# Performance work log

Measured on AMD Instinct MI355X. Metric: run time of the kernel, lower is better.

Reference implementation:

```python
import jax, jax.numpy as jnp
import numpy as np

B, R, D, P = 32, 512, 256, 5532  # images, rois/image, feat dim, num_pids
NEG_INF = -1e30

def setup_inputs() -> dict:
    key = jax.random.key(0)
    k1, k2, k3 = jax.random.split(key, 3)
    inputs = jax.random.normal(k1, (B * R, D), dtype=jnp.float32)
    cls_scores = jax.random.uniform(k2, (B * R, 1), dtype=jnp.float32)
    roi_label = jax.random.randint(k3, (B, R), 0, P + 1)  # 0 = background -> label -1
    return {"inputs": inputs, "cls_scores": cls_scores, "roi_label": roi_label}

def reference(inputs, cls_scores, roi_label):
    x = (inputs * cls_scores).reshape(B, R, D)          # scale features by cls score
    label = roi_label - 1                               # [B,R], -1 = background
    valid = label >= 0                                  # keep labeled ROIs only
    lbl = jnp.where(valid, label, 0)

    # per-image per-pid mean prototypes via one segmented reduction
    seg = (jnp.arange(B)[:, None] * P + lbl).reshape(-1)             # [B*R]
    w = valid.reshape(-1).astype(x.dtype)
    sums = jax.ops.segment_sum(x.reshape(-1, D) * w[:, None], seg, num_segments=B * P)
    counts = jax.ops.segment_sum(w, seg, num_segments=B * P)          # [B*P]
    proto = sums / jnp.maximum(counts, 1.0)[:, None]
    proto = proto / jnp.maximum(jnp.linalg.norm(proto, axis=-1, keepdims=True), 1e-12)
    proto = jax.lax.stop_gradient(proto).reshape(B, P, D)            # .detach() in torch
    present = (counts > 0).reshape(B, P)                              # unique labels per image

    # project each ROI feature onto its image's prototypes
    logits = jnp.einsum('brd,bpd->brp', x, proto)                     # [B,R,P]
    logits = jnp.where(present[:, None, :], logits, NEG_INF)          # softmax over unique labels only
    logp = jax.nn.log_softmax(logits, axis=-1)
    nll = -jnp.take_along_axis(logp, lbl[..., None], axis=-1)[..., 0] # [B,R]
    nll = jnp.where(valid, nll, 0.0)
    n_valid = jnp.maximum(jnp.sum(valid).astype(x.dtype), 1.0)
    return jnp.sum(nll) / n_valid
```

## Files before the change

kernel.cpp:

```cpp
#include <hip/hip_runtime.h>
#include <math.h>

#define Bn 32
#define Rn 512
#define Dn 256
#define Pn 5532
#define MAXU 512
#define NEGBIG -3.0e38f

typedef short short8 __attribute__((ext_vector_type(8)));
typedef short short4v __attribute__((ext_vector_type(4)));
typedef float floatx4 __attribute__((ext_vector_type(4)));

#define COUNTS_OFF   0
#define NLL_OFF      (Bn*Pn)
#define TICKET_OFF   (NLL_OFF + 1)
#define ZERO_WORDS   (TICKET_OFF + 3)
#define XBF_OFF      ZERO_WORDS
#define XBF_WORDS    (Bn*Rn*Dn/2)
#define PBF_OFF      (XBF_OFF + XBF_WORDS)
#define PBF_WORDS    (Bn*MAXU*Dn/2)
#define CMAP_OFF     (PBF_OFF + PBF_WORDS)
#define CCNT_OFF     (CMAP_OFF + Bn*Pn)
#define CURS_OFF     (CCNT_OFF + Bn*MAXU)
#define RLIST_OFF    (CURS_OFF + Bn*MAXU)
#define NUNIQ_OFF    (RLIST_OFF + Bn*Rn)
#define NVALID_OFF   (NUNIQ_OFF + 32)
#define MPART_OFF    (NVALID_OFF + 32)
#define SPART_OFF    (MPART_OFF + Bn*Rn*4)
#define DLBL_OFF     (SPART_OFF + Bn*Rn*4)

__device__ __forceinline__ unsigned short bf16r(float f) {
    union { float f; unsigned int u; } c; c.f = f;
    return (unsigned short)((c.u + 0x7FFFu + ((c.u >> 16) & 1u)) >> 16);
}

__device__ __forceinline__ void async16(void* lds, const void* g) {
    auto* l3 = reinterpret_cast<__attribute__((address_space(3))) unsigned int*>(
                   reinterpret_cast<size_t>(lds));
    auto* g1 = reinterpret_cast<const __attribute__((address_space(1))) unsigned int*>(
                   reinterpret_cast<size_t>(g));
    __builtin_amdgcn_global_load_lds(g1, l3, 16, 0, 0);
}

__global__ __launch_bounds__(256) void k_prep(const float* __restrict__ inputs,
                                              const float* __restrict__ cls,
                                              const int* __restrict__ roi_label,
                                              unsigned short* __restrict__ xbf,
                                              int* __restrict__ counts) {
    int i8 = blockIdx.x * 256 + threadIdx.x;
    if (i8 < Bn * Rn) {
        int b = i8 >> 9;
        int lbl = roi_label[i8] - 1;
        if (lbl >= 0) atomicAdd(&counts[b * Pn + lbl], 1);
    }
    int e = i8 * 8;
    int row = e >> 8;
    float cw = cls[row];
    float4 v0 = *(const float4*)&inputs[e];
    float4 v1 = *(const float4*)&inputs[e + 4];
    short8 o;
    o[0] = (short)bf16r(v0.x * cw); o[1] = (short)bf16r(v0.y * cw);
    o[2] = (short)bf16r(v0.z * cw); o[3] = (short)bf16r(v0.w * cw);
    o[4] = (short)bf16r(v1.x * cw); o[5] = (short)bf16r(v1.y * cw);
    o[6] = (short)bf16r(v1.z * cw); o[7] = (short)bf16r(v1.w * cw);
    *(short8*)&xbf[e] = o;
}

__global__ __launch_bounds__(1024) void k_compact(
    const int* __restrict__ roi_label, const int* __restrict__ counts,
    int* __restrict__ nuniq, int* __restrict__ cmap, int* __restrict__ ccnt,
    int* __restrict__ cursor, int* __restrict__ rlist, int* __restrict__ nvalid_arr) {
    const int b = blockIdx.x;
    const int t = threadIdx.x;
    const int lane = t & 63, wid = t >> 6;
    __shared__ int wpres[16], wcnt[16];
    __shared__ int cmap_lds[Pn];
    __shared__ int curs_lds[MAXU];
    int basePres = 0, baseCnt = 0;
    for (int i0 = 0; i0 < Pn; i0 += 1024) {
        int i = i0 + t;
        int cnt = (i < Pn) ? counts[b * Pn + i] : 0;
        bool pres = cnt > 0;
        unsigned long long mask = __ballot(pres);
        int pfx_pres = __popcll(mask & ((1ULL << lane) - 1ULL));
        int v = cnt;
        #pragma unroll
        for (int off = 1; off < 64; off <<= 1) {
            int u = __shfl_up(v, off);
            if (lane >= off) v += u;
        }
        int pfx_cnt = v - cnt;
        if (lane == 63) { wpres[wid] = __popcll(mask); wcnt[wid] = v; }
        __syncthreads();
        int woffP = 0, totP = 0, woffC = 0, totC = 0;
        #pragma unroll
        for (int w = 0; w < 16; ++w) {
            int p = wpres[w], c = wcnt[w];
            if (w < wid) { woffP += p; woffC += c; }
            totP += p; totC += c;
        }
        if (pres) {
            int c = basePres + woffP + pfx_pres;
            cmap_lds[i] = c;
            cmap[b * Pn + i] = c;
            ccnt[b * MAXU + c] = cnt;
            curs_lds[c] = baseCnt + woffC + pfx_cnt;
        }
        basePres += totP; baseCnt += totC;
        __syncthreads();
    }
    if (t < Rn) {
        int lbl = roi_label[b * Rn + t] - 1;
        if (lbl >= 0) {
            int c = cmap_lds[lbl];
            int pos = atomicAdd(&curs_lds[c], 1);
            rlist[b * Rn + pos] = t;
        }
    }
    __syncthreads();
    if (t < MAXU && t < basePres)
        cursor[b * MAXU + t] = curs_lds[t];
    if (t == 0) { nuniq[b] = basePres; nvalid_arr[b] = baseCnt; }
}

__global__ __launch_bounds__(64) void k_proto(
    const float* __restrict__ inputs, const float* __restrict__ cls,
    const int* __restrict__ nuniq, const int* __restrict__ ccnt,
    const int* __restrict__ cursor, const int* __restrict__ rlist,
    unsigned short* __restrict__ pbf) {
    int slot = blockIdx.x;
    int b = slot >> 9;
    int c = slot & (MAXU - 1);
    if (c >= nuniq[b]) return;
    int cnt = ccnt[slot];
    int start = cursor[slot] - cnt;
    int t = threadIdx.x;
    float4 acc = make_float4(0.f, 0.f, 0.f, 0.f);
    for (int k = 0; k < cnt; ++k) {
        int r = rlist[b * Rn + start + k];
        float cw = cls[b * Rn + r];
        float4 v = *(const float4*)&inputs[(size_t)(b * Rn + r) * Dn + t * 4];
        acc.x += v.x * cw; acc.y += v.y * cw; acc.z += v.z * cw; acc.w += v.w * cw;
    }
    float inv = 1.0f / (float)cnt;
    acc.x *= inv; acc.y *= inv; acc.z *= inv; acc.w *= inv;
    float ss = acc.x*acc.x + acc.y*acc.y + acc.z*acc.z + acc.w*acc.w;
    #pragma unroll
    for (int off = 32; off > 0; off >>= 1) ss += __shfl_xor(ss, off);
    float scale = 1.0f / fmaxf(sqrtf(ss), 1e-12f);
    short4v o;
    o[0] = (short)bf16r(acc.x * scale); o[1] = (short)bf16r(acc.y * scale);
    o[2] = (short)bf16r(acc.z * scale); o[3] = (short)bf16r(acc.w * scale);
    *(short4v*)&pbf[(size_t)slot * Dn + t * 4] = o;
}

#define TRr 128
#define TCc 128
#define KCk 32

__global__ __launch_bounds__(256, 3) void k_loss(
    const unsigned short* __restrict__ xbf, const unsigned short* __restrict__ pbf,
    const int* __restrict__ roi_label, const int* __restrict__ cmap,
    const int* __restrict__ nuniq,
    float* __restrict__ mpart, float* __restrict__ spart,
    float* __restrict__ dlbl_arr)
{
    __shared__ __align__(16) unsigned short xs[2][TRr * KCk];
    __shared__ __align__(16) unsigned short ps[2][TCc * KCk];
    __shared__ int lblc[TRr];
    __shared__ float mw[4][TRr], sw[4][TRr];

    const int t = threadIdx.x;
    const int lane = t & 63, w = t >> 6;
    const int q = lane >> 4, r15 = lane & 15;
    const int b = blockIdx.z;
    const int pc = blockIdx.y;
    const int roiBase = blockIdx.x * TRr;
    const int U = nuniq[b];
    if (pc * TCc >= U) return;

    if (t < TRr) {
        int lbl = roi_label[b * Rn + roiBase + t] - 1;
        lblc[t] = (lbl >= 0) ? cmap[b * Pn + lbl] : -1;
    }

    int xrow[2], xg[2], prow[2], pg[2];
    #pragma unroll
    for (int cc = 0; cc < 2; ++cc) {
        int s = (w + cc * 4) * 64 + lane;
        xrow[cc] = s >> 2; xg[cc] = (s & 3) ^ ((xrow[cc] >> 1) & 3);
        prow[cc] = s >> 2; pg[cc] = xg[cc];
    }

    #define ISSUE(kc, buf)                                                         \
        do {                                                                       \
            async16(&xs[buf][w * 512],                                             \
                    xbf + (size_t)(b * Rn + roiBase + xrow[0]) * Dn                \
                        + (kc) * KCk + xg[0] * 8);                                 \
            async16(&xs[buf][(w + 4) * 512],                                       \
                    xbf + (size_t)(b * Rn + roiBase + xrow[1]) * Dn                \
                        + (kc) * KCk + xg[1] * 8);                                 \
            async16(&ps[buf][w * 512],                                             \
                    pbf + (size_t)(b * MAXU + pc * TCc + prow[0]) * Dn             \
                        + (kc) * KCk + pg[0] * 8);                                 \
            async16(&ps[buf][(w + 4) * 512],                                       \
                    pbf + (size_t)(b * MAXU + pc * TCc + prow[1]) * Dn             \
                        + (kc) * KCk + pg[1] * 8);                                 \
        } while (0)

    ISSUE(0, 0);

    floatx4 acc[8][2];
    #pragma unroll
    for (int mt = 0; mt < 8; ++mt)
        #pragma unroll
        for (int nt = 0; nt < 2; ++nt) acc[mt][nt] = (floatx4)0.f;

    for (int kc = 0; kc < Dn / KCk; ++kc) {
        const int cur = kc & 1;
        __syncthreads();
        if (kc < Dn / KCk - 1) ISSUE(kc + 1, cur ^ 1);

        short8 bb[2];
        #pragma unroll
        for (int nt = 0; nt < 2; ++nt) {
            int row = w * 32 + nt * 16 + r15;
            int off = row * KCk + ((q ^ ((row >> 1) & 3)) * 8);
            bb[nt] = *(const short8*)&ps[cur][off];
        }
        #pragma unroll
        for (int mt = 0; mt < 8; ++mt) {
            int row = mt * 16 + r15;
            int off = row * KCk + ((q ^ ((row >> 1) & 3)) * 8);
            short8 a = *(const short8*)&xs[cur][off];
            acc[mt][0] = __builtin_amdgcn_mfma_f32_16x16x32_bf16(a, bb[0], acc[mt][0], 0, 0, 0);
            acc[mt][1] = __builtin_amdgcn_mfma_f32_16x16x32_bf16(a, bb[1], acc[mt][1], 0, 0, 0);
        }
    }

    const int c0 = pc * TCc + w * 32 + r15;
    const int c1 = c0 + 16;
    const bool v0 = c0 < U, v1 = c1 < U;
    #pragma unroll
    for (int mt = 0; mt < 8; ++mt)
        #pragma unroll
        for (int reg = 0; reg < 4; ++reg) {
            int mloc = mt * 16 + q * 4 + reg;
            float d0 = acc[mt][0][reg], d1 = acc[mt][1][reg];
            int lc = lblc[mloc];
            if (v0 && c0 == lc) dlbl_arr[b * Rn + roiBase + mloc] = d0;
            if (v1 && c1 == lc) dlbl_arr[b * Rn + roiBase + mloc] = d1;
            float M = fmaxf(v0 ? d0 : NEGBIG, v1 ? d1 : NEGBIG);
            #pragma unroll
            for (int off = 1; off < 16; off <<= 1) M = fmaxf(M, __shfl_xor(M, off));
            float s = (v0 ? __expf(d0 - M) : 0.f) + (v1 ? __expf(d1 - M) : 0.f);
            #pragma unroll
            for (int off = 1; off < 16; off <<= 1) s += __shfl_xor(s, off);
            if (r15 == 0) { mw[w][mloc] = M; sw[w][mloc] = s; }
        }
    __syncthreads();

    if (t < TRr) {
        float M = fmaxf(fmaxf(mw[0][t], mw[1][t]), fmaxf(mw[2][t], mw[3][t]));
        float s = 0.f;
        #pragma unroll
        for (int wv = 0; wv < 4; ++wv) s += sw[wv][t] * __expf(mw[wv][t] - M);
        int roi = b * Rn + roiBase + t;
        mpart[roi * 4 + pc] = M;
        spart[roi * 4 + pc] = s;
    }
    #undef ISSUE
}

__global__ __launch_bounds__(256) void k_merge(
    const int* __restrict__ roi_label, const int* __restrict__ nuniq,
    const float* __restrict__ mpart, const float* __restrict__ spart,
    const float* __restrict__ dlbl_arr, float* __restrict__ nll_sum,
    int* __restrict__ ticket, const int* __restrict__ nvalid_arr,
    float* __restrict__ out)
{
    __shared__ float wsum[4];
    int roi = blockIdx.x * 256 + threadIdx.x;
    int b = roi >> 9;
    int lbl = roi_label[roi] - 1;
    float v = 0.f;
    if (lbl >= 0) {
        int U = nuniq[b];
        int nch = (U + TCc - 1) / TCc;
        float m = NEGBIG, s = 0.f;
        for (int pc = 0; pc < nch; ++pc) {
            float om = mpart[roi * 4 + pc], os = spart[roi * 4 + pc];
            float M = fmaxf(m, om);
            s = s * __expf(m - M) + os * __expf(om - M);
            m = M;
        }
        v = m + __logf(s) - dlbl_arr[roi];
    }
    #pragma unroll
    for (int off = 1; off < 64; off <<= 1) v += __shfl_xor(v, off);
    int lane = threadIdx.x & 63, wid = threadIdx.x >> 6;
    if (lane == 0) wsum[wid] = v;
    __syncthreads();
    if (threadIdx.x == 0) {
        atomicAdd(nll_sum, wsum[0] + wsum[1] + wsum[2] + wsum[3]);
        __threadfence();
        int tk = atomicAdd(ticket, 1);
        if (tk == gridDim.x - 1) {
            __threadfence();
            int s = 0;
            #pragma unroll
            for (int bb = 0; bb < Bn; ++bb) s += nvalid_arr[bb];
            out[0] = nll_sum[0] / fmaxf((float)s, 1.0f);
        }
    }
}

extern "C" void kernel_launch(void* const* d_in, const int* in_sizes, int n_in,
                              void* d_out, int out_size, void* d_ws, size_t ws_size,
                              hipStream_t stream) {
    const float* inputs = (const float*)d_in[0];
    const float* cls    = (const float*)d_in[1];
    const int*   roi    = (const int*)d_in[2];
    float* out = (float*)d_out;

    float* wsf = (float*)d_ws;
    int*   wsi = (int*)d_ws;
    int*   counts = wsi + COUNTS_OFF;
    float* nll    = wsf + NLL_OFF;
    int*   ticket = wsi + TICKET_OFF;
    unsigned short* xbf = (unsigned short*)(wsi + XBF_OFF);
    unsigned short* pbf = (unsigned short*)(wsi + PBF_OFF);
    int*   cmap   = wsi + CMAP_OFF;
    int*   ccnt   = wsi + CCNT_OFF;
    int*   cursor = wsi + CURS_OFF;
    int*   rlist  = wsi + RLIST_OFF;
    int*   nuniq  = wsi + NUNIQ_OFF;
    int*   nvalid = wsi + NVALID_OFF;
    float* mpart  = wsf + MPART_OFF;
    float* spart  = wsf + SPART_OFF;
    float* dlbl   = wsf + DLBL_OFF;

    hipMemsetAsync(d_ws, 0, (size_t)ZERO_WORDS * 4, stream);
    k_prep   <<<(Bn*Rn*Dn)/(256*8), 256, 0, stream>>>(inputs, cls, roi, xbf, counts);
    k_compact<<<Bn, 1024, 0, stream>>>(roi, counts, nuniq, cmap, ccnt, cursor, rlist, nvalid);
    k_proto  <<<Bn*MAXU, 64, 0, stream>>>(inputs, cls, nuniq, ccnt, cursor, rlist, pbf);
    dim3 g(Rn / TRr, 4, Bn);
    k_loss   <<<g, 256, 0, stream>>>(xbf, pbf, roi, cmap, nuniq, mpart, spart, dlbl);
    k_merge  <<<(Bn*Rn)/256, 256, 0, stream>>>(roi, nuniq, mpart, spart, dlbl, nll,
                                               ticket, nvalid, out);
}
```

Measured before the change: 115.6 us.

## Fuse prep and compaction, drop memset and atomics, single-block final merge

Merges the bf16 conversion and label compaction into one launch. Compaction blocks now count labels in LDS instead of through global atomics, so the hipMemset of the counts array goes away. The proto kernel processes 8 slots per block to cut block count. The merge becomes a single 1024-thread block that reduces without atomics or a ticket. Removing two launches and the memset should shrink fixed overhead, but the single-block merge serializes 16K ROIs onto one CU and the fused kernel uses large LDS for its conversion blocks.

```diff
diff --git a/kernel.cpp b/kernel.cpp
--- a/kernel.cpp
+++ b/kernel.cpp
@@ -12,23 +12,19 @@
 typedef short short4v __attribute__((ext_vector_type(4)));
 typedef float floatx4 __attribute__((ext_vector_type(4)));
 
-#define COUNTS_OFF   0
-#define NLL_OFF      (Bn*Pn)
-#define TICKET_OFF   (NLL_OFF + 1)
-#define ZERO_WORDS   (TICKET_OFF + 3)
-#define XBF_OFF      ZERO_WORDS
-#define XBF_WORDS    (Bn*Rn*Dn/2)
-#define PBF_OFF      (XBF_OFF + XBF_WORDS)
-#define PBF_WORDS    (Bn*MAXU*Dn/2)
-#define CMAP_OFF     (PBF_OFF + PBF_WORDS)
-#define CCNT_OFF     (CMAP_OFF + Bn*Pn)
-#define CURS_OFF     (CCNT_OFF + Bn*MAXU)
-#define RLIST_OFF    (CURS_OFF + Bn*MAXU)
-#define NUNIQ_OFF    (RLIST_OFF + Bn*Rn)
-#define NVALID_OFF   (NUNIQ_OFF + 32)
-#define MPART_OFF    (NVALID_OFF + 32)
-#define SPART_OFF    (MPART_OFF + Bn*Rn*4)
-#define DLBL_OFF     (SPART_OFF + Bn*Rn*4)
+#define XBF_OFF    0
+#define XBF_WORDS  (Bn*Rn*Dn/2)
+#define PBF_OFF    (XBF_OFF + XBF_WORDS)
+#define PBF_WORDS  (Bn*MAXU*Dn/2)
+#define CMAP_OFF   (PBF_OFF + PBF_WORDS)
+#define CCNT_OFF   (CMAP_OFF + Bn*Pn)
+#define CURS_OFF   (CCNT_OFF + Bn*MAXU)
+#define RLIST_OFF  (CURS_OFF + Bn*MAXU)
+#define NUNIQ_OFF  (RLIST_OFF + Bn*Rn)
+#define NVALID_OFF (NUNIQ_OFF + 32)
+#define MPART_OFF  (NVALID_OFF + 32)
+#define SPART_OFF  (MPART_OFF + Bn*Rn*4)
+#define DLBL_OFF   (SPART_OFF + Bn*Rn*4)
 
 __device__ __forceinline__ unsigned short bf16r(float f) {
     union { float f; unsigned int u; } c; c.f = f;
@@ -43,44 +39,51 @@
     __builtin_amdgcn_global_load_lds(g1, l3, 16, 0, 0);
 }
 
-__global__ __launch_bounds__(256) void k_prep(const float* __restrict__ inputs,
-                                              const float* __restrict__ cls,
-                                              const int* __restrict__ roi_label,
-                                              unsigned short* __restrict__ xbf,
-                                              int* __restrict__ counts) {
-    int i8 = blockIdx.x * 256 + threadIdx.x;
-    if (i8 < Bn * Rn) {
-        int b = i8 >> 9;
-        int lbl = roi_label[i8] - 1;
-        if (lbl >= 0) atomicAdd(&counts[b * Pn + lbl], 1);
-    }
-    int e = i8 * 8;
-    int row = e >> 8;
-    float cw = cls[row];
-    float4 v0 = *(const float4*)&inputs[e];
-    float4 v1 = *(const float4*)&inputs[e + 4];
-    short8 o;
-    o[0] = (short)bf16r(v0.x * cw); o[1] = (short)bf16r(v0.y * cw);
-    o[2] = (short)bf16r(v0.z * cw); o[3] = (short)bf16r(v0.w * cw);
-    o[4] = (short)bf16r(v1.x * cw); o[5] = (short)bf16r(v1.y * cw);
-    o[6] = (short)bf16r(v1.z * cw); o[7] = (short)bf16r(v1.w * cw);
-    *(short8*)&xbf[e] = o;
-}
-
-__global__ __launch_bounds__(1024) void k_compact(
-    const int* __restrict__ roi_label, const int* __restrict__ counts,
-    int* __restrict__ nuniq, int* __restrict__ cmap, int* __restrict__ ccnt,
-    int* __restrict__ cursor, int* __restrict__ rlist, int* __restrict__ nvalid_arr) {
-    const int b = blockIdx.x;
+__global__ __launch_bounds__(1024) void k1_prep_compact(
+    const float* __restrict__ inputs, const float* __restrict__ cls,
+    const int* __restrict__ roi_label,
+    unsigned short* __restrict__ xbf,
+    int* __restrict__ cmap, int* __restrict__ ccnt, int* __restrict__ cursor,
+    int* __restrict__ rlist, int* __restrict__ nuniq, int* __restrict__ nvalid_arr)
+{
+    const int flat = blockIdx.x;
     const int t = threadIdx.x;
-    const int lane = t & 63, wid = t >> 6;
-    __shared__ int wpres[16], wcnt[16];
+
+    __shared__ int cnt_lds[Pn];
     __shared__ int cmap_lds[Pn];
     __shared__ int curs_lds[MAXU];
+    __shared__ int wpres[16], wcnt[16];
+
+    if (flat >= 32) {
+        int g = (flat - 32) * 1024 + t;
+        int e = g * 8;
+        int row = e >> 8;
+        float cw = cls[row];
+        float4 v0 = *(const float4*)&inputs[e];
+        float4 v1 = *(const float4*)&inputs[e + 4];
+        short8 o;
+        o[0] = (short)bf16r(v0.x * cw); o[1] = (short)bf16r(v0.y * cw);
+        o[2] = (short)bf16r(v0.z * cw); o[3] = (short)bf16r(v0.w * cw);
+        o[4] = (short)bf16r(v1.x * cw); o[5] = (short)bf16r(v1.y * cw);
+        o[6] = (short)bf16r(v1.z * cw); o[7] = (short)bf16r(v1.w * cw);
+        *(short8*)&xbf[e] = o;
+        return;
+    }
+
+    const int b = flat;
+    const int lane = t & 63, wid = t >> 6;
+    for (int i = t; i < Pn; i += 1024) cnt_lds[i] = 0;
+    __syncthreads();
+    if (t < Rn) {
+        int lbl = roi_label[b * Rn + t] - 1;
+        if (lbl >= 0) atomicAdd(&cnt_lds[lbl], 1);
+    }
+    __syncthreads();
+
     int basePres = 0, baseCnt = 0;
     for (int i0 = 0; i0 < Pn; i0 += 1024) {
         int i = i0 + t;
-        int cnt = (i < Pn) ? counts[b * Pn + i] : 0;
+        int cnt = (i < Pn) ? cnt_lds[i] : 0;
         bool pres = cnt > 0;
         unsigned long long mask = __ballot(pres);
         int pfx_pres = __popcll(mask & ((1ULL << lane) - 1ULL));
@@ -124,42 +127,45 @@
     if (t == 0) { nuniq[b] = basePres; nvalid_arr[b] = baseCnt; }
 }
 
-__global__ __launch_bounds__(64) void k_proto(
+__global__ __launch_bounds__(64) void k2_proto(
     const float* __restrict__ inputs, const float* __restrict__ cls,
     const int* __restrict__ nuniq, const int* __restrict__ ccnt,
     const int* __restrict__ cursor, const int* __restrict__ rlist,
-    unsigned short* __restrict__ pbf) {
-    int slot = blockIdx.x;
-    int b = slot >> 9;
-    int c = slot & (MAXU - 1);
-    if (c >= nuniq[b]) return;
-    int cnt = ccnt[slot];
-    int start = cursor[slot] - cnt;
+    unsigned short* __restrict__ pbf)
+{
     int t = threadIdx.x;
-    float4 acc = make_float4(0.f, 0.f, 0.f, 0.f);
-    for (int k = 0; k < cnt; ++k) {
-        int r = rlist[b * Rn + start + k];
-        float cw = cls[b * Rn + r];
-        float4 v = *(const float4*)&inputs[(size_t)(b * Rn + r) * Dn + t * 4];
-        acc.x += v.x * cw; acc.y += v.y * cw; acc.z += v.z * cw; acc.w += v.w * cw;
-    }
-    float inv = 1.0f / (float)cnt;
-    acc.x *= inv; acc.y *= inv; acc.z *= inv; acc.w *= inv;
-    float ss = acc.x*acc.x + acc.y*acc.y + acc.z*acc.z + acc.w*acc.w;
-    #pragma unroll
-    for (int off = 32; off > 0; off >>= 1) ss += __shfl_xor(ss, off);
-    float scale = 1.0f / fmaxf(sqrtf(ss), 1e-12f);
-    short4v o;
-    o[0] = (short)bf16r(acc.x * scale); o[1] = (short)bf16r(acc.y * scale);
-    o[2] = (short)bf16r(acc.z * scale); o[3] = (short)bf16r(acc.w * scale);
-    *(short4v*)&pbf[(size_t)slot * Dn + t * 4] = o;
+    int s0 = blockIdx.x * 8;
+    for (int s = s0; s < s0 + 8; ++s) {
+        int b = s >> 9;
+        int c = s & (MAXU - 1);
+        if (c >= nuniq[b]) continue;
+        int cnt = ccnt[s];
+        int start = cursor[s] - cnt;
+        float4 acc = make_float4(0.f, 0.f, 0.f, 0.f);
+        for (int k = 0; k < cnt; ++k) {
+            int r = rlist[b * Rn + start + k];
+            float cw = cls[b * Rn + r];
+            float4 v = *(const float4*)&inputs[(size_t)(b * Rn + r) * Dn + t * 4];
+            acc.x += v.x * cw; acc.y += v.y * cw; acc.z += v.z * cw; acc.w += v.w * cw;
+        }
+        float inv = 1.0f / (float)cnt;
+        acc.x *= inv; acc.y *= inv; acc.z *= inv; acc.w *= inv;
+        float ss = acc.x*acc.x + acc.y*acc.y + acc.z*acc.z + acc.w*acc.w;
+        #pragma unroll
+        for (int off = 32; off > 0; off >>= 1) ss += __shfl_xor(ss, off);
+        float scale = 1.0f / fmaxf(sqrtf(ss), 1e-12f);
+        short4v o;
+        o[0] = (short)bf16r(acc.x * scale); o[1] = (short)bf16r(acc.y * scale);
+        o[2] = (short)bf16r(acc.z * scale); o[3] = (short)bf16r(acc.w * scale);
+        *(short4v*)&pbf[(size_t)s * Dn + t * 4] = o;
+    }
 }
 
 #define TRr 128
 #define TCc 128
 #define KCk 32
 
-__global__ __launch_bounds__(256, 3) void k_loss(
+__global__ __launch_bounds__(256, 3) void k3_loss(
     const unsigned short* __restrict__ xbf, const unsigned short* __restrict__ pbf,
     const int* __restrict__ roi_label, const int* __restrict__ cmap,
     const int* __restrict__ nuniq,
@@ -185,12 +191,11 @@
         lblc[t] = (lbl >= 0) ? cmap[b * Pn + lbl] : -1;
     }
 
-    int xrow[2], xg[2], prow[2], pg[2];
+    int xrow[2], xg[2];
     #pragma unroll
     for (int cc = 0; cc < 2; ++cc) {
         int s = (w + cc * 4) * 64 + lane;
         xrow[cc] = s >> 2; xg[cc] = (s & 3) ^ ((xrow[cc] >> 1) & 3);
-        prow[cc] = s >> 2; pg[cc] = xg[cc];
     }
 
     #define ISSUE(kc, buf)                                                         \
@@ -202,11 +207,11 @@
                     xbf + (size_t)(b * Rn + roiBase + xrow[1]) * Dn                \
                         + (kc) * KCk + xg[1] * 8);                                 \
             async16(&ps[buf][w * 512],                                             \
-                    pbf + (size_t)(b * MAXU + pc * TCc + prow[0]) * Dn             \
-                        + (kc) * KCk + pg[0] * 8);                                 \
+                    pbf + (size_t)(b * MAXU + pc * TCc + xrow[0]) * Dn             \
+                        + (kc) * KCk + xg[0] * 8);                                 \
             async16(&ps[buf][(w + 4) * 512],                                       \
-                    pbf + (size_t)(b * MAXU + pc * TCc + prow[1]) * Dn             \
-                        + (kc) * KCk + pg[1] * 8);                                 \
+                    pbf + (size_t)(b * MAXU + pc * TCc + xrow[1]) * Dn             \
+                        + (kc) * KCk + xg[1] * 8);                                 \
         } while (0)
 
     ISSUE(0, 0);
@@ -238,6 +243,7 @@
             acc[mt][1] = __builtin_amdgcn_mfma_f32_16x16x32_bf16(a, bb[1], acc[mt][1], 0, 0, 0);
         }
     }
+    #undef ISSUE
 
     const int c0 = pc * TCc + w * 32 + r15;
     const int c1 = c0 + 16;
@@ -270,49 +276,46 @@
         mpart[roi * 4 + pc] = M;
         spart[roi * 4 + pc] = s;
     }
-    #undef ISSUE
-}
-
-__global__ __launch_bounds__(256) void k_merge(
+}
+
+__global__ __launch_bounds__(1024) void k4_merge(
     const int* __restrict__ roi_label, const int* __restrict__ nuniq,
     const float* __restrict__ mpart, const float* __restrict__ spart,
-    const float* __restrict__ dlbl_arr, float* __restrict__ nll_sum,
-    int* __restrict__ ticket, const int* __restrict__ nvalid_arr,
+    const float* __restrict__ dlbl_arr, const int* __restrict__ nvalid_arr,
     float* __restrict__ out)
 {
-    __shared__ float wsum[4];
-    int roi = blockIdx.x * 256 + threadIdx.x;
-    int b = roi >> 9;
-    int lbl = roi_label[roi] - 1;
+    __shared__ float wsum[16];
+    const int t = threadIdx.x;
+    const int lane = t & 63, wid = t >> 6;
     float v = 0.f;
-    if (lbl >= 0) {
-        int U = nuniq[b];
-        int nch = (U + TCc - 1) / TCc;
-        float m = NEGBIG, s = 0.f;
-        for (int pc = 0; pc < nch; ++pc) {
-            float om = mpart[roi * 4 + pc], os = spart[roi * 4 + pc];
-            float M = fmaxf(m, om);
-            s = s * __expf(m - M) + os * __expf(om - M);
-            m = M;
-        }
-        v = m + __logf(s) - dlbl_arr[roi];
+    for (int roi = t; roi < Bn * Rn; roi += 1024) {
+        int b = roi >> 9;
+        int lbl = roi_label[roi] - 1;
+        if (lbl >= 0) {
+            int U = nuniq[b];
+            int nch = (U + TCc - 1) / TCc;
+            float m = NEGBIG, s = 0.f;
+            for (int pc = 0; pc < nch; ++pc) {
+                float om = mpart[roi * 4 + pc], os = spart[roi * 4 + pc];
+                float M = fmaxf(m, om);
+                s = s * __expf(m - M) + os * __expf(om - M);
+                m = M;
+            }
+            v += m + __logf(s) - dlbl_arr[roi];
+        }
     }
     #pragma unroll
     for (int off = 1; off < 64; off <<= 1) v += __shfl_xor(v, off);
-    int lane = threadIdx.x & 63, wid = threadIdx.x >> 6;
     if (lane == 0) wsum[wid] = v;
     __syncthreads();
-    if (threadIdx.x == 0) {
-        atomicAdd(nll_sum, wsum[0] + wsum[1] + wsum[2] + wsum[3]);
-        __threadfence();
-        int tk = atomicAdd(ticket, 1);
-        if (tk == gridDim.x - 1) {
-            __threadfence();
-            int s = 0;
-            #pragma unroll
-            for (int bb = 0; bb < Bn; ++bb) s += nvalid_arr[bb];
-            out[0] = nll_sum[0] / fmaxf((float)s, 1.0f);
-        }
+    if (t < 64) {
+        float x = (t < 16) ? wsum[t] : 0.f;
+        #pragma unroll
+        for (int off = 1; off < 64; off <<= 1) x += __shfl_xor(x, off);
+        int nv = (t < Bn) ? nvalid_arr[t] : 0;
+        #pragma unroll
+        for (int off = 1; off < 64; off <<= 1) nv += __shfl_xor(nv, off);
+        if (t == 0) out[0] = x / fmaxf((float)nv, 1.0f);
     }
 }
 
@@ -326,9 +329,6 @@
 
     float* wsf = (float*)d_ws;
     int*   wsi = (int*)d_ws;
-    int*   counts = wsi + COUNTS_OFF;
-    float* nll    = wsf + NLL_OFF;
-    int*   ticket = wsi + TICKET_OFF;
     unsigned short* xbf = (unsigned short*)(wsi + XBF_OFF);
     unsigned short* pbf = (unsigned short*)(wsi + PBF_OFF);
     int*   cmap   = wsi + CMAP_OFF;
@@ -341,12 +341,11 @@
     float* spart  = wsf + SPART_OFF;
     float* dlbl   = wsf + DLBL_OFF;
 
-    hipMemsetAsync(d_ws, 0, (size_t)ZERO_WORDS * 4, stream);
-    k_prep   <<<(Bn*Rn*Dn)/(256*8), 256, 0, stream>>>(inputs, cls, roi, xbf, counts);
-    k_compact<<<Bn, 1024, 0, stream>>>(roi, counts, nuniq, cmap, ccnt, cursor, rlist, nvalid);
-    k_proto  <<<Bn*MAXU, 64, 0, stream>>>(inputs, cls, nuniq, ccnt, cursor, rlist, pbf);
+    k1_prep_compact<<<32 + 512, 1024, 0, stream>>>(inputs, cls, roi, xbf, cmap, ccnt,
+                                                   cursor, rlist, nuniq, nvalid);
+    k2_proto<<<(Bn * MAXU) / 8, 64, 0, stream>>>(inputs, cls, nuniq, ccnt, cursor,
+                                                 rlist, pbf);
     dim3 g(Rn / TRr, 4, Bn);
-    k_loss   <<<g, 256, 0, stream>>>(xbf, pbf, roi, cmap, nuniq, mpart, spart, dlbl);
-    k_merge  <<<(Bn*Rn)/256, 256, 0, stream>>>(roi, nuniq, mpart, spart, dlbl, nll,
-                                               ticket, nvalid, out);
-}
+    k3_loss<<<g, 256, 0, stream>>>(xbf, pbf, roi, cmap, nuniq, mpart, spart, dlbl);
+    k4_merge<<<1, 1024, 0, stream>>>(roi, nuniq, mpart, spart, dlbl, nvalid, out);
+}
```

After: 146.5 us. +26.7%, slower.
